# Kernel tuning notes

Measured on AMD Instinct MI355X. Metric: run time of the kernel, lower is better.

Reference implementation:

```python
import jax, jax.numpy as jnp
import numpy as np

GRID = 1024   # grid side -> V = GRID^2 verts
BATCH = 8     # homogeneous batch of meshes


def _grid_mesh_faces(S):
    # Triangulated regular grid: 2 triangles per cell.
    idx = np.arange(S * S, dtype=np.int64).reshape(S, S)
    a = idx[:-1, :-1].ravel()
    b = a + 1
    c = a + S
    d = a + S + 1
    f1 = np.stack([a, b, c], axis=1)
    f2 = np.stack([b, d, c], axis=1)
    return np.concatenate([f1, f2], axis=0)  # (F, 3) int64


def _unique_edges(faces, V):
    # Edge k of a face is opposite vertex k (pytorch3d convention):
    # edges = [(v1,v2), (v0,v2), (v0,v1)]
    e = np.stack([faces[:, [1, 2]], faces[:, [0, 2]], faces[:, [0, 1]]], axis=1)  # (F,3,2)
    e = np.sort(e, axis=-1)
    keys = e[..., 0] * np.int64(V) + e[..., 1]
    uniq, inv = np.unique(keys.ravel(), return_inverse=True)
    edges = np.stack([uniq // V, uniq % V], axis=1).astype(np.int64)  # (E,2)
    face_to_edge = inv.reshape(-1, 3).astype(np.int64)                # (F,3)
    return edges, face_to_edge


def setup_inputs() -> dict:
    key = jax.random.key(0)
    V = GRID * GRID
    faces_np = _grid_mesh_faces(GRID)
    edges_np, fte_np = _unique_edges(faces_np, V)
    verts = jax.random.normal(key, (BATCH, V, 3), dtype=jnp.float32)
    return {
        "verts": verts,
        "faces": jnp.asarray(faces_np),
        "edges": jnp.asarray(edges_np),
        "face_to_edge": jnp.asarray(fte_np),
    }


def reference(verts, faces, edges, face_to_edge):
    # verts: (N, V, 3); faces: (F, 3); edges: (E, 2); face_to_edge: (F, 3)
    N, V, _ = verts.shape
    # Gather edge endpoints and average to midpoints: (N, E, 2, 3) -> (N, E, 3)
    mid = verts[:, edges].mean(axis=2)
    # New verts = original verts followed by edge midpoints
    new_verts = jnp.concatenate([verts, mid], axis=1)  # (N, V+E, 3)
    # New faces (pytorch3d SubdivideMeshes._subdivide_faces ordering):
    e = face_to_edge + V  # midpoint vertex indices
    f0 = jnp.stack([faces[:, 0], e[:, 2], e[:, 1]], axis=1)
    f1 = jnp.stack([faces[:, 1], e[:, 0], e[:, 2]], axis=1)
    f2 = jnp.stack([faces[:, 2], e[:, 1], e[:, 0]], axis=1)
    f3 = e
    new_faces = jnp.concatenate([f0, f1, f2, f3], axis=0)  # (4F, 3)
    return new_verts, new_faces
```

## Files before the change

kernel.cpp:

```cpp
#include <hip/hip_runtime.h>
#include <stdint.h>


#define GRID_S 1024
#define V_CONST (GRID_S * GRID_S)
#define PER_BATCH (V_CONST * 3)
#define CHUNKS_PER_BATCH (PER_BATCH / 4 / 256)

typedef float f4v __attribute__((ext_vector_type(4)));
typedef float f2v __attribute__((ext_vector_type(2)));

__device__ __forceinline__ void store12(float* p, f4v w0, f4v w1, f4v w2) {
    const uintptr_t a = (uintptr_t)p;
    if ((a & 15) == 0) {
        f4v* q = reinterpret_cast<f4v*>(p);
        q[0] = w0; q[1] = w1; q[2] = w2;
    } else if ((a & 7) == 0) {
        f2v* q = reinterpret_cast<f2v*>(p);
        q[0] = (f2v){w0[0], w0[1]};
        q[1] = (f2v){w0[2], w0[3]};
        q[2] = (f2v){w1[0], w1[1]};
        q[3] = (f2v){w1[2], w1[3]};
        q[4] = (f2v){w2[0], w2[1]};
        q[5] = (f2v){w2[2], w2[3]};
    } else {
#pragma unroll
        for (int i = 0; i < 4; ++i) p[i] = w0[i];
#pragma unroll
        for (int i = 0; i < 4; ++i) p[4 + i] = w1[i];
#pragma unroll
        for (int i = 0; i < 4; ++i) p[8 + i] = w2[i];
    }
}

__global__ __launch_bounds__(256) void fused_k(
    const float* __restrict__ verts,
    const int2*  __restrict__ edges,
    const int*   __restrict__ faces,
    const int*   __restrict__ fte,
    float* __restrict__ out,
    int E, int F, int N, int rowStride3, int baseOut,
    int Bcopy, int Bmid) {

    const int b = blockIdx.x;
    const int tid = threadIdx.x;

    if (b < Bcopy) {
        const int n  = b / CHUNKS_PER_BATCH;
        const int cb = b - n * CHUNKS_PER_BATCH;
        const int d0 = n * rowStride3;
        const float* __restrict__ src = verts + n * PER_BATCH;
        float* __restrict__ dst = out + d0;
        const int pad = (4 - (d0 & 3)) & 3;
        const int main4 = (PER_BATCH - pad) >> 2;
        const int k = cb * 256 + tid;
        if (k < main4) {
            const int s = pad + (k << 2);
            f4v v;
            if (pad == 0) {
                v = *reinterpret_cast<const f4v*>(src + s);
            } else {
                v[0] = src[s + 0];
                v[1] = src[s + 1];
                v[2] = src[s + 2];
                v[3] = src[s + 3];
            }
            *reinterpret_cast<f4v*>(dst + s) = v;
        }
        if (k == 0) {
            const int rem = (PER_BATCH - pad) & 3;
            for (int i = 0; i < pad; ++i) dst[i] = src[i];
            for (int i = PER_BATCH - rem; i < PER_BATCH; ++i) dst[i] = src[i];
        }
        return;
    }

    if (b < Bcopy + Bmid) {
        const int e = (b - Bcopy) * 256 + tid;
        if (e >= E) return;
        const int2 ed = edges[e];
        const int i0 = 3 * ed.x;
        const int i1 = 3 * ed.y;
        const float* __restrict__ vb = verts;
        float* __restrict__ o = out + (V_CONST + e) * 3;
#pragma unroll 2
        for (int n = 0; n < N; ++n) {
            const float x = 0.5f * (vb[i0 + 0] + vb[i1 + 0]);
            const float y = 0.5f * (vb[i0 + 1] + vb[i1 + 1]);
            const float z = 0.5f * (vb[i0 + 2] + vb[i1 + 2]);
            o[0] = x; o[1] = y; o[2] = z;
            vb += PER_BATCH;
            o  += rowStride3;
        }
        return;
    }

    const int t = (b - Bcopy - Bmid) * 256 + tid;
    const int mainT = F >> 2;
    float* __restrict__ base = out + baseOut;

    if (t < mainT) {
        const int4* f4 = reinterpret_cast<const int4*>(faces) + 3 * t;
        const int4* q4 = reinterpret_cast<const int4*>(fte) + 3 * t;
        const int4 p0 = f4[0], p1 = f4[1], p2 = f4[2];
        const int4 q0 = q4[0], q1 = q4[1], q2 = q4[2];

        const float a0 = (float)p0.x, a1 = (float)p0.w, a2 = (float)p1.z, a3 = (float)p2.y;
        const float b0 = (float)p0.y, b1 = (float)p1.x, b2 = (float)p1.w, b3 = (float)p2.z;
        const float c0 = (float)p0.z, c1 = (float)p1.y, c2 = (float)p2.x, c3 = (float)p2.w;

        const float e00 = (float)(q0.x + V_CONST), e01 = (float)(q0.w + V_CONST),
                    e02 = (float)(q1.z + V_CONST), e03 = (float)(q2.y + V_CONST);
        const float e10 = (float)(q0.y + V_CONST), e11 = (float)(q1.x + V_CONST),
                    e12 = (float)(q1.w + V_CONST), e13 = (float)(q2.z + V_CONST);
        const float e20 = (float)(q0.z + V_CONST), e21 = (float)(q1.y + V_CONST),
                    e22 = (float)(q2.x + V_CONST), e23 = (float)(q2.w + V_CONST);

        const int off = 12 * t;
        const int segF = 3 * F;

        store12(base + off,
                (f4v){a0, e20, e10, a1}, (f4v){e21, e11, a2, e22}, (f4v){e12, a3, e23, e13});
        store12(base + segF + off,
                (f4v){b0, e00, e20, b1}, (f4v){e01, e21, b2, e02}, (f4v){e22, b3, e03, e23});
        store12(base + 2 * segF + off,
                (f4v){c0, e10, e00, c1}, (f4v){e11, e01, c2, e12}, (f4v){e02, c3, e13, e03});
        store12(base + 3 * segF + off,
                (f4v){e00, e10, e20, e01}, (f4v){e11, e21, e02, e12}, (f4v){e22, e03, e13, e23});
    } else if (t == mainT) {
        for (int f = mainT * 4; f < F; ++f) {
            const int a = faces[3 * f + 0];
            const int bb = faces[3 * f + 1];
            const int c = faces[3 * f + 2];
            const int e0 = fte[3 * f + 0] + V_CONST;
            const int e1 = fte[3 * f + 1] + V_CONST;
            const int e2 = fte[3 * f + 2] + V_CONST;
            float* o0 = base + 3 * f;
            float* o1 = o0 + 3 * F;
            float* o2 = o1 + 3 * F;
            float* o3 = o2 + 3 * F;
            o0[0] = (float)a;  o0[1] = (float)e2; o0[2] = (float)e1;
            o1[0] = (float)bb; o1[1] = (float)e0; o1[2] = (float)e2;
            o2[0] = (float)c;  o2[1] = (float)e1; o2[2] = (float)e0;
            o3[0] = (float)e0; o3[1] = (float)e1; o3[2] = (float)e2;
        }
    }
}

extern "C" void kernel_launch(void* const* d_in, const int* in_sizes, int n_in,
                              void* d_out, int out_size, void* d_ws, size_t ws_size,
                              hipStream_t stream) {
    const float* verts = (const float*)d_in[0];
    const int* faces   = (const int*)d_in[1];
    const int* edges   = (const int*)d_in[2];
    const int* fte     = (const int*)d_in[3];
    float* out = (float*)d_out;

    const int F = in_sizes[1] / 3;
    const int E = in_sizes[2] / 2;
    const int N = in_sizes[0] / (V_CONST * 3);

    const int rowStride3 = (V_CONST + E) * 3;
    const int baseOut    = N * rowStride3;

    const int Bcopy = N * CHUNKS_PER_BATCH;
    const int Bmid  = (E + 255) / 256;
    const int Bfac  = ((F >> 2) + 1 + 255) / 256;
    const int blocks = Bcopy + Bmid + Bfac;

    fused_k<<<blocks, 256, 0, stream>>>(verts, (const int2*)edges, faces, fte,
                                        out, E, F, N, rowStride3, baseOut,
                                        Bcopy, Bmid);
}
```

Before: 650.1 us.

## Stage vertex copy and midpoint stores through LDS for aligned vector writes

The vertex-copy blocks now each handle 4096 floats. They load them with aligned float4 reads into shared memory and write them back out as aligned float4 stores shifted by the destination pad, replacing scalar loads when the pad is nonzero. The midpoint blocks first compute all 8 batches in registers, then stage each batch's 768 floats through LDS so they go out as coalesced float4 stores instead of strided 3-float scalar stores. This trades extra __syncthreads barriers and 16KB of LDS per block, which may cut occupancy, for fewer and wider global memory transactions.

```diff
diff --git a/kernel.cpp b/kernel.cpp
--- a/kernel.cpp
+++ b/kernel.cpp
@@ -5,7 +5,7 @@
 #define GRID_S 1024
 #define V_CONST (GRID_S * GRID_S)
 #define PER_BATCH (V_CONST * 3)
-#define CHUNKS_PER_BATCH (PER_BATCH / 4 / 256)
+#define CPB 768
 
 typedef float f4v __attribute__((ext_vector_type(4)));
 typedef float f2v __attribute__((ext_vector_type(2)));
@@ -42,55 +42,112 @@
     int E, int F, int N, int rowStride3, int baseOut,
     int Bcopy, int Bmid) {
 
+    __shared__ float lds[4100];
     const int b = blockIdx.x;
     const int tid = threadIdx.x;
 
     if (b < Bcopy) {
-        const int n  = b / CHUNKS_PER_BATCH;
-        const int cb = b - n * CHUNKS_PER_BATCH;
+        const int n  = b / CPB;
+        const int cb = b - n * CPB;
         const int d0 = n * rowStride3;
         const float* __restrict__ src = verts + n * PER_BATCH;
         float* __restrict__ dst = out + d0;
         const int pad = (4 - (d0 & 3)) & 3;
         const int main4 = (PER_BATCH - pad) >> 2;
-        const int k = cb * 256 + tid;
-        if (k < main4) {
-            const int s = pad + (k << 2);
-            f4v v;
-            if (pad == 0) {
-                v = *reinterpret_cast<const f4v*>(src + s);
-            } else {
-                v[0] = src[s + 0];
-                v[1] = src[s + 1];
-                v[2] = src[s + 2];
-                v[3] = src[s + 3];
-            }
-            *reinterpret_cast<f4v*>(dst + s) = v;
-        }
-        if (k == 0) {
+        const int sBase = cb * 4096;
+
+#pragma unroll
+        for (int j = 0; j < 4; ++j) {
+            const int o = 1024 * j + 4 * tid;
+            *reinterpret_cast<f4v*>(&lds[o]) =
+                *reinterpret_cast<const f4v*>(src + sBase + o);
+        }
+        if (pad && tid < 3) {
+            const int si = sBase + 4096 + tid;
+            lds[4096 + tid] = (si < PER_BATCH) ? src[si] : 0.0f;
+        }
+        __syncthreads();
+
+#pragma unroll
+        for (int j = 0; j < 4; ++j) {
+            const int loc = 1024 * j + 4 * tid;
+            const int k4 = cb * 1024 + (loc >> 2);
+            if (k4 < main4) {
+                f4v v;
+                if (pad == 0) {
+                    v = *reinterpret_cast<const f4v*>(&lds[loc]);
+                } else {
+                    v[0] = lds[loc + pad + 0];
+                    v[1] = lds[loc + pad + 1];
+                    v[2] = lds[loc + pad + 2];
+                    v[3] = lds[loc + pad + 3];
+                }
+                *reinterpret_cast<f4v*>(dst + pad + 4 * k4) = v;
+            }
+        }
+        if (cb == 0 && tid == 0) {
+            for (int i = 0; i < pad; ++i) dst[i] = src[i];
             const int rem = (PER_BATCH - pad) & 3;
-            for (int i = 0; i < pad; ++i) dst[i] = src[i];
             for (int i = PER_BATCH - rem; i < PER_BATCH; ++i) dst[i] = src[i];
         }
         return;
     }
 
     if (b < Bcopy + Bmid) {
-        const int e = (b - Bcopy) * 256 + tid;
-        if (e >= E) return;
-        const int2 ed = edges[e];
-        const int i0 = 3 * ed.x;
-        const int i1 = 3 * ed.y;
-        const float* __restrict__ vb = verts;
-        float* __restrict__ o = out + (V_CONST + e) * 3;
-#pragma unroll 2
-        for (int n = 0; n < N; ++n) {
-            const float x = 0.5f * (vb[i0 + 0] + vb[i1 + 0]);
-            const float y = 0.5f * (vb[i0 + 1] + vb[i1 + 1]);
-            const float z = 0.5f * (vb[i0 + 2] + vb[i1 + 2]);
-            o[0] = x; o[1] = y; o[2] = z;
-            vb += PER_BATCH;
-            o  += rowStride3;
+        const int blk = b - Bcopy;
+        const int e0 = blk << 8;
+        const int e  = e0 + tid;
+
+        if ((e0 + 256 <= E) && (N == 8)) {
+            const int2 ed = edges[e];
+            const int i0 = 3 * ed.x;
+            const int i1 = 3 * ed.y;
+            float mx[8], my[8], mz[8];
+            const float* __restrict__ vb = verts;
+#pragma unroll
+            for (int n = 0; n < 8; ++n) {
+                mx[n] = 0.5f * (vb[i0 + 0] + vb[i1 + 0]);
+                my[n] = 0.5f * (vb[i0 + 1] + vb[i1 + 1]);
+                mz[n] = 0.5f * (vb[i0 + 2] + vb[i1 + 2]);
+                vb += PER_BATCH;
+            }
+            const int gb = (V_CONST + e0) * 3;
+#pragma unroll
+            for (int n = 0; n < 8; ++n) {
+                if (n) __syncthreads();
+                lds[3 * tid + 0] = mx[n];
+                lds[3 * tid + 1] = my[n];
+                lds[3 * tid + 2] = mz[n];
+                __syncthreads();
+                const int g0 = gb + n * rowStride3;
+                const int head = (4 - (g0 & 3)) & 3;
+                const int m4 = (768 - head) >> 2;
+                if (tid < m4) {
+                    const int l = head + (tid << 2);
+                    f4v v;
+                    v[0] = lds[l + 0]; v[1] = lds[l + 1];
+                    v[2] = lds[l + 2]; v[3] = lds[l + 3];
+                    *reinterpret_cast<f4v*>(out + g0 + l) = v;
+                } else if (tid == m4) {
+                    for (int j = 0; j < head; ++j) out[g0 + j] = lds[j];
+                    const int tail = (768 - head) & 3;
+                    for (int j = 0; j < tail; ++j)
+                        out[g0 + 768 - tail + j] = lds[768 - tail + j];
+                }
+            }
+        } else if (e < E) {
+            const int2 ed = edges[e];
+            const int i0 = 3 * ed.x;
+            const int i1 = 3 * ed.y;
+            const float* __restrict__ vb = verts;
+            float* __restrict__ o = out + (V_CONST + e) * 3;
+            for (int n = 0; n < N; ++n) {
+                o[0] = 0.5f * (vb[i0 + 0] + vb[i1 + 0]);
+                o[1] = 0.5f * (vb[i0 + 1] + vb[i1 + 1]);
+                o[2] = 0.5f * (vb[i0 + 2] + vb[i1 + 2]);
+                vb += PER_BATCH;
+                o  += rowStride3;
+            }
         }
         return;
     }
@@ -163,7 +220,7 @@
     const int rowStride3 = (V_CONST + E) * 3;
     const int baseOut    = N * rowStride3;
 
-    const int Bcopy = N * CHUNKS_PER_BATCH;
+    const int Bcopy = N * CPB;
     const int Bmid  = (E + 255) / 256;
     const int Bfac  = ((F >> 2) + 1 + 255) / 256;
     const int blocks = Bcopy + Bmid + Bfac;
```

After: 663.9 us. +2.1%, slower.
